# Performance work log

Measured on AMD Instinct MI355X. Metric: run time of the kernel, lower is better.

Reference implementation:

```python
import jax, jax.numpy as jnp
import numpy as np

N, E, IN, H, F = 50000, 800000, 128, 4, 32
NEG_SLOPE = 0.2


def setup_inputs() -> dict:
    key = jax.random.key(0)
    ks = jax.random.split(key, 10)
    feat = jax.random.normal(ks[0], (N, IN), dtype=jnp.float32)
    s = 0.05  # small scale to keep activations stable
    W_src_mut = jax.random.normal(ks[1], (IN, H * F), dtype=jnp.float32) * s
    W_dst_mut = jax.random.normal(ks[2], (IN, H * F), dtype=jnp.float32) * s
    W_self = jax.random.normal(ks[3], (IN, H * F), dtype=jnp.float32) * s
    W_lin = jax.random.normal(ks[4], (IN, F), dtype=jnp.float32) * s
    attn = jax.random.normal(ks[5], (H, F), dtype=jnp.float32) * s
    src = jax.random.randint(ks[6], (E,), 0, N, dtype=jnp.int64)
    dst = jax.random.randint(ks[7], (E,), 0, N, dtype=jnp.int64)
    return {
        'feat': feat,
        'W_src_mut': W_src_mut, 'b_src_mut': jnp.zeros((H * F,), jnp.float32),
        'W_dst_mut': W_dst_mut, 'b_dst_mut': jnp.zeros((H * F,), jnp.float32),
        'W_self': W_self, 'b_self': jnp.zeros((H * F,), jnp.float32),
        'W_lin': W_lin, 'b_lin': jnp.zeros((F,), jnp.float32),
        'attn': attn, 'src': src, 'dst': dst,
    }


def reference(feat, W_src_mut, b_src_mut, W_dst_mut, b_dst_mut,
              W_self, b_self, W_lin, b_lin, attn, src, dst):
    n = feat.shape[0]
    # node projections -> [N, H, F]
    el_mut = (feat @ W_src_mut + b_src_mut).reshape(n, H, F)
    er_mut = (feat @ W_dst_mut + b_dst_mut).reshape(n, H, F)
    el_self = (feat @ W_self + b_self).reshape(n, H, F)
    feat_lin = (feat @ W_lin + b_lin)[:, None, :]  # [N, 1, F]
    # edge attention scores: u_add_v -> leaky_relu -> dot with attn -> [E, H]
    e = jax.nn.leaky_relu(el_mut[src] + er_mut[dst], NEG_SLOPE)
    s = jnp.einsum('ehf,hf->eh', e, attn)
    # edge softmax over incoming edges of each dst node
    smax = jax.ops.segment_max(s, dst, num_segments=n)
    ex = jnp.exp(s - smax[dst])
    denom = jax.ops.segment_sum(ex, dst, num_segments=n)
    a = ex / denom[dst]  # [E, H]
    # weighted aggregation: u_mul_e + sum over dst
    m = el_self[src] * a[:, :, None]  # [E, H, F]
    ft = jax.ops.segment_sum(m, dst, num_segments=n)  # [N, H, F]
    # concat along head axis: [N, H+1, F]
    return jnp.concatenate([feat_lin, ft], axis=1)
```

## Files before the change

### kernel.cpp

```cpp
#include <hip/hip_runtime.h>
#include <hip/hip_bf16.h>

#define NN 50000
#define EE 800000
#define INF_ 128
#define HH 4
#define FF 32
#define HF 128
#define OUTC 160
#define NEG_SLOPE 0.2f

#define CAP 64
#define CSTRIDE 16

typedef __attribute__((ext_vector_type(8))) short short8;
typedef __attribute__((ext_vector_type(4))) float f32x4;
typedef _Float16 f16x2 __attribute__((ext_vector_type(2)));
typedef float fl2 __attribute__((ext_vector_type(2)));

__device__ __forceinline__ unsigned short f2bf(float f) {
    union { float f; unsigned u; } in; in.f = f;
    unsigned u = in.u;
    u += 0x7fffu + ((u >> 16) & 1u);
    return (unsigned short)(u >> 16);
}
__device__ __forceinline__ unsigned short f2h(float f) {
    _Float16 h = (_Float16)f;
    return __builtin_bit_cast(unsigned short, h);
}
__device__ __forceinline__ f16x2 bch(unsigned u) {
    return __builtin_bit_cast(f16x2, u);
}
__device__ __forceinline__ f16x2 habs2(f16x2 v) {
    unsigned u = __builtin_bit_cast(unsigned, v) & 0x7FFF7FFFu;
    return __builtin_bit_cast(f16x2, u);
}

__device__ __forceinline__ void async_cp16(const void* g, void* l) {
    __builtin_amdgcn_global_load_lds(
        (const __attribute__((address_space(1))) void*)g,
        (__attribute__((address_space(3))) void*)l, 16, 0, 0);
}

__global__ __launch_bounds__(256) void prep_w(
    const float* __restrict__ W0, const float* __restrict__ b0,
    const float* __restrict__ W1, const float* __restrict__ b1,
    const float* __restrict__ W2, const float* __restrict__ b2,
    const float* __restrict__ W3, const float* __restrict__ b3,
    const float* __restrict__ attn,
    unsigned short* __restrict__ WbT, float* __restrict__ biasc,
    unsigned short* __restrict__ ath, int* __restrict__ counts)
{
    int idx = blockIdx.x * 256 + threadIdx.x;
    if (idx < NN) {
        uint4 z = make_uint4(0, 0, 0, 0);
        uint4* p = (uint4*)(counts + (size_t)idx * CSTRIDE);
        p[0] = z; p[1] = z; p[2] = z; p[3] = z;
    }
    int n = idx >> 7, k = idx & 127;
    float v;
    if (n < 256) {
        int g = n >> 3, j = n & 7;
        int ch = g * 4 + (j & 3);
        v = (j < 4) ? W0[k * 128 + ch] : W2[k * 128 + ch];
    } else if (n < 384) {
        v = W1[k * 128 + (n - 256)];
    } else {
        v = W3[k * 32 + (n - 384)];
    }
    int phys = (((k >> 3) ^ (n & 15)) << 3) | (k & 7);
    WbT[n * 128 + phys] = f2bf(v);
    if (idx < 416) {
        float bv;
        if (idx < 256) {
            int g = idx >> 3, j = idx & 7;
            int ch = g * 4 + (j & 3);
            bv = (j < 4) ? b0[ch] : b2[ch];
        } else if (idx < 384) {
            bv = b1[idx - 256];
        } else {
            bv = b3[idx - 384];
        }
        biasc[idx] = bv;
    }
    if (idx < 128) ath[idx] = f2h(attn[idx]);
}


template<int CPR, int CSTR, int CA0>
__device__ __forceinline__ void copy_out(
    const unsigned short* Cs, int row0, int tid,
    unsigned short* __restrict__ ms, unsigned short* __restrict__ erh)
{
    for (int c = tid; c < 64 * CPR; c += 256) {
        int row = c / CPR, c16 = c - row * CPR;
        int grow = row0 + row;
        if (grow >= NN) continue;
        uint4 v = *(const uint4*)(Cs + row * CSTR + c16 * 8);
        int ca = CA0 + c16;
        if (ca < 32) *(uint4*)(ms  + (size_t)grow * 256 + ca * 8) = v;
        else         *(uint4*)(erh + (size_t)grow * 128 + (ca - 32) * 8) = v;
    }
}

__global__ __launch_bounds__(256) void gemm_hist(
    const float* __restrict__ feat,
    const unsigned short* __restrict__ WbT,
    const float* __restrict__ biasc,
    const int* __restrict__ src, const int* __restrict__ dst,
    unsigned short* __restrict__ ms, unsigned short* __restrict__ erh,
    float* __restrict__ out,
    int* __restrict__ counts, int* __restrict__ srcbuck)
{
    __shared__ __align__(16) char lds[16384 + 28672];
    unsigned short* As = (unsigned short*)lds;
    unsigned short* Bs = (unsigned short*)(lds + 16384);
    unsigned short* Cs = (unsigned short*)lds;

    const int tid  = threadIdx.x;
    const int wv   = tid >> 6;
    const int lane = tid & 63;
    const int row0 = blockIdx.x * 64;
    const int yb   = blockIdx.y;

    const int e = (yb * 782 + blockIdx.x) * 256 + tid;
    int ed = 0, es = 0;
    if (e < EE) { ed = dst[e]; es = src[e]; }
    asm volatile("" :: "v"(ed), "v"(es));

    const int ntile = (yb & 1) ? 6 : 7;
    const int base  = (yb == 0) ? 0 : (yb == 1) ? 112 : (yb == 2) ? 208 : 320;

    {
        const char* g = (const char*)(WbT + (size_t)base * 128);
        #pragma unroll
        for (int it = 0; it < 7; ++it) {
            if (it < ntile) {
                int seg = wv * ntile + it;
                async_cp16(g + seg * 1024 + lane * 16, (char*)Bs + seg * 1024);
            }
        }
    }
    {
        #pragma unroll
        for (int i = 0; i < 4; ++i) {
            int idx = i * 256 + tid;
            int r = idx >> 4, c = idx & 15;
            int grow = row0 + r;
            float4 v0 = make_float4(0.f, 0.f, 0.f, 0.f), v1 = v0;
            if (grow < NN) {
                const float4* fp = (const float4*)(feat + (size_t)grow * 128 + c * 8);
                v0 = fp[0]; v1 = fp[1];
            }
            uint4 o;
            o.x = (unsigned)f2bf(v0.x) | ((unsigned)f2bf(v0.y) << 16);
            o.y = (unsigned)f2bf(v0.z) | ((unsigned)f2bf(v0.w) << 16);
            o.z = (unsigned)f2bf(v1.x) | ((unsigned)f2bf(v1.y) << 16);
            o.w = (unsigned)f2bf(v1.z) | ((unsigned)f2bf(v1.w) << 16);
            *(uint4*)(As + r * 128 + ((c ^ (r & 15)) << 3)) = o;
        }
    }
    __syncthreads();

    const int m16  = lane & 15;
    const int quad = lane >> 4;

    f32x4 acc[7];
    #pragma unroll
    for (int t = 0; t < 7; ++t) acc[t] = (f32x4){0.f, 0.f, 0.f, 0.f};

    short8 afr[4];
    {
        const unsigned short* Ab = As + (wv * 16 + m16) * 128;
        #pragma unroll
        for (int ks = 0; ks < 4; ++ks)
            afr[ks] = *(const short8*)(Ab + (((ks * 4 + quad) ^ m16) << 3));
    }

    #pragma unroll
    for (int t = 0; t < 7; ++t) {
        if (t >= ntile) break;
        const unsigned short* Bb = Bs + (t * 16 + m16) * 128;
        #pragma unroll
        for (int ks = 0; ks < 4; ++ks) {
            short8 bfr = *(const short8*)(Bb + (((ks * 4 + quad) ^ m16) << 3));
            acc[t] = __builtin_amdgcn_mfma_f32_16x16x32_bf16(afr[ks], bfr, acc[t], 0, 0, 0);
        }
    }

    if (yb == 3) {
        #pragma unroll
        for (int t = 4; t < 6; ++t) {
            int col = 320 + t * 16 + m16;
            float bb = biasc[col];
            #pragma unroll
            for (int r = 0; r < 4; ++r) {
                int grow = row0 + wv * 16 + quad * 4 + r;
                if (grow < NN) out[(size_t)grow * OUTC + (col - 384)] = acc[t][r] + bb;
            }
        }
    }

    __syncthreads();

    const int ntf  = (yb == 3) ? 4 : ntile;
    const int cstr = (yb & 1) ? ((yb == 1) ? 104 : 72) : 120;
    #pragma unroll
    for (int t = 0; t < 7; ++t) {
        if (t >= ntf) break;
        int col = base + t * 16 + m16;
        float bb = biasc[col];
        #pragma unroll
        for (int r = 0; r < 4; ++r) {
            int lrow = wv * 16 + quad * 4 + r;
            Cs[lrow * cstr + t * 16 + m16] = f2h(acc[t][r] + bb);
        }
    }
    __syncthreads();

    if (yb == 0)      copy_out<14, 120, 0 >(Cs, row0, tid, ms, erh);
    else if (yb == 1) copy_out<12, 104, 14>(Cs, row0, tid, ms, erh);
    else if (yb == 2) copy_out<14, 120, 26>(Cs, row0, tid, ms, erh);
    else              copy_out<8,  72,  40>(Cs, row0, tid, ms, erh);

    if (e < EE) {
        int r = atomicAdd(&counts[(size_t)ed * CSTRIDE], 1);
        if (r < CAP) srcbuck[(size_t)ed * CAP + r] = es;
    }
}

__device__ __forceinline__ void edgeP(
    const uint4 v, const f16x2 er01, const f16x2 er23,
    const f16x2 at01, const f16x2 at23,
    float& l, float& a0, float& a1, float& a2, float& a3)
{
    f16x2 z01 = bch(v.x) + er01;
    f16x2 z23 = bch(v.y) + er23;
    float s1 = __builtin_amdgcn_fdot2(at01, z01, 0.f, false);
    s1 = __builtin_amdgcn_fdot2(at23, z23, s1, false);
    float s2 = __builtin_amdgcn_fdot2(at01, habs2(z01), 0.f, false);
    s2 = __builtin_amdgcn_fdot2(at23, habs2(z23), s2, false);
    float s = fmaf(0.6f, s1, 0.4f * s2);
    s += __shfl_xor(s, 1, 64);
    s += __shfl_xor(s, 2, 64);
    s += __shfl_xor(s, 4, 64);
    float p = __expf(s);
    l += p;
    fl2 c01 = __builtin_convertvector(bch(v.z), fl2);
    fl2 c23 = __builtin_convertvector(bch(v.w), fl2);
    a0 = fmaf(p, c01.x, a0);
    a1 = fmaf(p, c01.y, a1);
    a2 = fmaf(p, c23.x, a2);
    a3 = fmaf(p, c23.y, a3);
}

__global__ __launch_bounds__(256) void node_agg8(
    const unsigned short* __restrict__ ms,
    const unsigned short* __restrict__ erh,
    const unsigned short* __restrict__ ath,
    const int* __restrict__ counts,
    const int* __restrict__ srcbuck,
    float* __restrict__ out)
{
    const int n = blockIdx.x * 4 + (threadIdx.x >> 6);
    if (n >= NN) return;
    const int lane = threadIdx.x & 63;
    const int half = lane >> 5;
    const int li   = lane & 31;

    uint2 aw = *(const uint2*)(ath + li * 4);
    uint2 ew = *(const uint2*)(erh + (size_t)n * HF + li * 4);
    const f16x2 at01 = bch(aw.x), at23 = bch(aw.y);
    const f16x2 er01 = bch(ew.x), er23 = bch(ew.y);

    const int beg = n * CAP;
    int deg = counts[(size_t)n * CSTRIDE];
    deg = (deg > CAP) ? CAP : deg;
    const int cnt0 = (deg + 1) >> 1;
    const int st  = beg + (half ? cnt0 : 0);
    const int cnt = half ? (deg - cnt0) : cnt0;

    float l = 0.f, a0 = 0.f, a1 = 0.f, a2 = 0.f, a3 = 0.f;

    int k = 0;
    for (; k + 4 <= cnt; k += 4) {
        int i0 = srcbuck[st + k];
        int i1 = srcbuck[st + k + 1];
        int i2 = srcbuck[st + k + 2];
        int i3 = srcbuck[st + k + 3];
        uint4 v0 = *(const uint4*)(ms + (size_t)i0 * 256 + li * 8);
        uint4 v1 = *(const uint4*)(ms + (size_t)i1 * 256 + li * 8);
        uint4 v2 = *(const uint4*)(ms + (size_t)i2 * 256 + li * 8);
        uint4 v3 = *(const uint4*)(ms + (size_t)i3 * 256 + li * 8);
        edgeP(v0, er01, er23, at01, at23, l, a0, a1, a2, a3);
        edgeP(v1, er01, er23, at01, at23, l, a0, a1, a2, a3);
        edgeP(v2, er01, er23, at01, at23, l, a0, a1, a2, a3);
        edgeP(v3, er01, er23, at01, at23, l, a0, a1, a2, a3);
    }
    for (; k < cnt; ++k) {
        int i0 = srcbuck[st + k];
        uint4 v0 = *(const uint4*)(ms + (size_t)i0 * 256 + li * 8);
        edgeP(v0, er01, er23, at01, at23, l, a0, a1, a2, a3);
    }

    l  += __shfl_xor(l,  32, 64);
    a0 += __shfl_xor(a0, 32, 64);
    a1 += __shfl_xor(a1, 32, 64);
    a2 += __shfl_xor(a2, 32, 64);
    a3 += __shfl_xor(a3, 32, 64);

    if (half == 0) {
        float inv = (l > 0.f) ? __frcp_rn(l) : 0.f;
        float4 r = make_float4(a0 * inv, a1 * inv, a2 * inv, a3 * inv);
        *(float4*)(out + (size_t)n * OUTC + FF + li * 4) = r;
    }
}

extern "C" void kernel_launch(void* const* d_in, const int* in_sizes, int n_in,
                              void* d_out, int out_size, void* d_ws, size_t ws_size,
                              hipStream_t stream) {
    const float* feat   = (const float*)d_in[0];
    const float* W_src  = (const float*)d_in[1];
    const float* b_src  = (const float*)d_in[2];
    const float* W_dst  = (const float*)d_in[3];
    const float* b_dst  = (const float*)d_in[4];
    const float* W_self = (const float*)d_in[5];
    const float* b_self = (const float*)d_in[6];
    const float* W_lin  = (const float*)d_in[7];
    const float* b_lin  = (const float*)d_in[8];
    const float* attn   = (const float*)d_in[9];
    const int*   src    = (const int*)d_in[10];
    const int*   dst    = (const int*)d_in[11];
    float* out = (float*)d_out;

    unsigned short* ms    = (unsigned short*)d_ws;
    unsigned short* erh   = ms  + (size_t)NN * 256;
    unsigned short* WbT   = erh + (size_t)NN * HF;
    unsigned short* ath   = WbT + 416 * 128;
    float* biasc   = (float*)(ath + 128);
    int*   counts  = (int*)(biasc + 416);
    int*   srcbuck = counts + (size_t)NN * CSTRIDE;

    prep_w<<<208, 256, 0, stream>>>(W_src, b_src, W_dst, b_dst, W_self, b_self,
                                    W_lin, b_lin, attn, WbT, biasc, ath, counts);

    {
        dim3 grid(782, 4);
        gemm_hist<<<grid, 256, 0, stream>>>(feat, WbT, biasc, src, dst,
                                            ms, erh, out, counts, srcbuck);
    }

    node_agg8<<<(NN + 3) / 4, 256, 0, stream>>>(ms, erh, ath,
                                                counts, srcbuck, out);
}
```

Measured before the change: 203.4 us.

## Load edge indices once per wave and double-buffer neighbor gathers

The aggregation kernel now loads all 64 bucketed source indices for a node with one coalesced load per wave and hands them to lanes with shuffles, replacing the scalar index loads made inside the loop. The edge loop becomes a two-stage software pipeline: the next group of four neighbor rows is fetched while the current group is processed. Tail edges are clamped to a valid index and masked by zeroing their weight. This aims to hide gather latency and remove the dependent index-then-data load chain, at the cost of more registers and some wasted loads on padded slots.

```diff
diff --git a/kernel.cpp b/kernel.cpp
--- a/kernel.cpp
+++ b/kernel.cpp
@@ -229,8 +229,19 @@
     }
 }
 
-__device__ __forceinline__ void edgeP(
-    const uint4 v, const f16x2 er01, const f16x2 er23,
+
+__device__ __forceinline__ int bgeti(int idxv, int stL, int cnt, int k) {
+    int kk = (k < cnt) ? k : (cnt - 1);
+    return __shfl(idxv, stL + kk, 64);
+}
+__device__ __forceinline__ uint4 ldms(const unsigned short* __restrict__ ms,
+                                      int i, int li) {
+    return *(const uint4*)(ms + (size_t)i * 256 + li * 8);
+}
+
+__device__ __forceinline__ void edgeM(
+    const uint4 v, const bool valid,
+    const f16x2 er01, const f16x2 er23,
     const f16x2 at01, const f16x2 at23,
     float& l, float& a0, float& a1, float& a2, float& a3)
 {
@@ -244,7 +255,7 @@
     s += __shfl_xor(s, 1, 64);
     s += __shfl_xor(s, 2, 64);
     s += __shfl_xor(s, 4, 64);
-    float p = __expf(s);
+    float p = valid ? __expf(s) : 0.f;
     l += p;
     fl2 c01 = __builtin_convertvector(bch(v.z), fl2);
     fl2 c23 = __builtin_convertvector(bch(v.w), fl2);
@@ -254,7 +265,7 @@
     a3 = fmaf(p, c23.y, a3);
 }
 
-__global__ __launch_bounds__(256) void node_agg8(
+__global__ __launch_bounds__(256) void node_agg9(
     const unsigned short* __restrict__ ms,
     const unsigned short* __restrict__ erh,
     const unsigned short* __restrict__ ath,
@@ -268,39 +279,55 @@
     const int half = lane >> 5;
     const int li   = lane & 31;
 
+    const int idxv = srcbuck[n * CAP + lane];
+    int deg = counts[(size_t)n * CSTRIDE];
+    deg = (deg > CAP) ? CAP : deg;
+
     uint2 aw = *(const uint2*)(ath + li * 4);
     uint2 ew = *(const uint2*)(erh + (size_t)n * HF + li * 4);
     const f16x2 at01 = bch(aw.x), at23 = bch(aw.y);
     const f16x2 er01 = bch(ew.x), er23 = bch(ew.y);
 
-    const int beg = n * CAP;
-    int deg = counts[(size_t)n * CSTRIDE];
-    deg = (deg > CAP) ? CAP : deg;
     const int cnt0 = (deg + 1) >> 1;
-    const int st  = beg + (half ? cnt0 : 0);
-    const int cnt = half ? (deg - cnt0) : cnt0;
+    const int stL  = half ? cnt0 : 0;
+    const int cnt  = half ? (deg - cnt0) : cnt0;
 
     float l = 0.f, a0 = 0.f, a1 = 0.f, a2 = 0.f, a3 = 0.f;
 
-    int k = 0;
-    for (; k + 4 <= cnt; k += 4) {
-        int i0 = srcbuck[st + k];
-        int i1 = srcbuck[st + k + 1];
-        int i2 = srcbuck[st + k + 2];
-        int i3 = srcbuck[st + k + 3];
-        uint4 v0 = *(const uint4*)(ms + (size_t)i0 * 256 + li * 8);
-        uint4 v1 = *(const uint4*)(ms + (size_t)i1 * 256 + li * 8);
-        uint4 v2 = *(const uint4*)(ms + (size_t)i2 * 256 + li * 8);
-        uint4 v3 = *(const uint4*)(ms + (size_t)i3 * 256 + li * 8);
-        edgeP(v0, er01, er23, at01, at23, l, a0, a1, a2, a3);
-        edgeP(v1, er01, er23, at01, at23, l, a0, a1, a2, a3);
-        edgeP(v2, er01, er23, at01, at23, l, a0, a1, a2, a3);
-        edgeP(v3, er01, er23, at01, at23, l, a0, a1, a2, a3);
-    }
-    for (; k < cnt; ++k) {
-        int i0 = srcbuck[st + k];
-        uint4 v0 = *(const uint4*)(ms + (size_t)i0 * 256 + li * 8);
-        edgeP(v0, er01, er23, at01, at23, l, a0, a1, a2, a3);
+    if (cnt > 0) {
+        const int nb = (cnt + 3) >> 2;
+        uint4 A0 = ldms(ms, bgeti(idxv, stL, cnt, 0), li);
+        uint4 A1 = ldms(ms, bgeti(idxv, stL, cnt, 1), li);
+        uint4 A2 = ldms(ms, bgeti(idxv, stL, cnt, 2), li);
+        uint4 A3 = ldms(ms, bgeti(idxv, stL, cnt, 3), li);
+        for (int b = 0; b < nb; b += 2) {
+            const int kB = (b + 1) * 4;
+            const bool hasB = (b + 1) < nb;
+            uint4 B0, B1, B2, B3;
+            if (hasB) {
+                B0 = ldms(ms, bgeti(idxv, stL, cnt, kB + 0), li);
+                B1 = ldms(ms, bgeti(idxv, stL, cnt, kB + 1), li);
+                B2 = ldms(ms, bgeti(idxv, stL, cnt, kB + 2), li);
+                B3 = ldms(ms, bgeti(idxv, stL, cnt, kB + 3), li);
+            }
+            const int kA = b * 4;
+            edgeM(A0, kA + 0 < cnt, er01, er23, at01, at23, l, a0, a1, a2, a3);
+            edgeM(A1, kA + 1 < cnt, er01, er23, at01, at23, l, a0, a1, a2, a3);
+            edgeM(A2, kA + 2 < cnt, er01, er23, at01, at23, l, a0, a1, a2, a3);
+            edgeM(A3, kA + 3 < cnt, er01, er23, at01, at23, l, a0, a1, a2, a3);
+            if (!hasB) break;
+            const int kN = (b + 2) * 4;
+            if (b + 2 < nb) {
+                A0 = ldms(ms, bgeti(idxv, stL, cnt, kN + 0), li);
+                A1 = ldms(ms, bgeti(idxv, stL, cnt, kN + 1), li);
+                A2 = ldms(ms, bgeti(idxv, stL, cnt, kN + 2), li);
+                A3 = ldms(ms, bgeti(idxv, stL, cnt, kN + 3), li);
+            }
+            edgeM(B0, kB + 0 < cnt, er01, er23, at01, at23, l, a0, a1, a2, a3);
+            edgeM(B1, kB + 1 < cnt, er01, er23, at01, at23, l, a0, a1, a2, a3);
+            edgeM(B2, kB + 2 < cnt, er01, er23, at01, at23, l, a0, a1, a2, a3);
+            edgeM(B3, kB + 3 < cnt, er01, er23, at01, at23, l, a0, a1, a2, a3);
+        }
     }
 
     l  += __shfl_xor(l,  32, 64);
@@ -350,6 +377,6 @@
                                             ms, erh, out, counts, srcbuck);
     }
 
-    node_agg8<<<(NN + 3) / 4, 256, 0, stream>>>(ms, erh, ath,
+    node_agg9<<<(NN + 3) / 4, 256, 0, stream>>>(ms, erh, ath,
                                                 counts, srcbuck, out);
 }
```

New measurement: 202.8 us. About the same (-0.3%).
